# Performance work log

Hardware: AMD Instinct MI355X
Metric: run time of the kernel (lower is better)

## Reference

```python
import jax, jax.numpy as jnp
import numpy as np

B = 4096           # batch size
NG = 4096          # num_gene_sets (columns of input)
G = 1024           # number of aggregation groups
GS = 32            # members per group (CSR-packed; code handles ragged too)
T = G * GS         # total flat indices


def setup_inputs() -> dict:
    key = jax.random.key(0)
    k1, k2, k3 = jax.random.split(key, 3)
    gene_set_features = jax.random.normal(k1, (B, NG), dtype=jnp.float32)
    att_weights = jax.random.normal(k2, (T,), dtype=jnp.float32)  # concat of per-group logits
    flat_idx = jax.random.randint(k3, (T,), 0, NG, dtype=jnp.int64)
    segment_ids = (jnp.arange(T, dtype=jnp.int64) // GS)          # sorted group id per entry
    return {
        "gene_set_features": gene_set_features,
        "att_weights": att_weights,
        "flat_idx": flat_idx,
        "segment_ids": segment_ids,
        "num_segments": G,
    }


def reference(gene_set_features, att_weights, flat_idx, segment_ids, num_segments):
    # Per-group (segment) softmax over the batch-independent attention logits.
    seg_max = jax.ops.segment_max(att_weights, segment_ids, num_segments=num_segments)
    ex = jnp.exp(att_weights - seg_max[segment_ids])
    denom = jax.ops.segment_sum(ex, segment_ids, num_segments=num_segments)
    attn = ex / denom[segment_ids]                     # (T,) softmax weights per group
    # Gather all group members for every batch row in one shot, weight, segment-sum.
    gathered = gene_set_features[:, flat_idx]          # (B, T)
    weighted = gathered * attn[None, :]                # (B, T)
    out = jax.ops.segment_sum(weighted.T, segment_ids, num_segments=num_segments).T  # (B, G)
    return out
```

## Files before the change

kernel.cpp:

```cpp
#include <hip/hip_runtime.h>

#define NGK 4096
#define BK 4096
#define GK 1024
#define GSK 32
#define TK (GK * GSK)

#define BTILE 4
#define AGG_THREADS 512

__global__ __launch_bounds__(256) void seg_softmax_kernel(
        const float* __restrict__ att,
        const int*   __restrict__ idx,
        unsigned*    __restrict__ pairs) {
    int t = blockIdx.x * 256 + threadIdx.x;
    float w = att[t];

    float m = w;
    #pragma unroll
    for (int d = 16; d >= 1; d >>= 1) m = fmaxf(m, __shfl_xor(m, d, 32));
    float e = expf(w - m);
    float s = e;
    #pragma unroll
    for (int d = 16; d >= 1; d >>= 1) s += __shfl_xor(s, d, 32);

    unsigned uw = __float_as_uint(e / s);
    uw = (uw + 0x7fffu + ((uw >> 16) & 1u)) & 0xffff0000u;

    int g = t >> 5;
    int j = t & 31;
    pairs[((j >> 2) * GK + g) * 4 + (j & 3)] = uw | ((unsigned)idx[t] << 4);
}

__global__ __launch_bounds__(AGG_THREADS, 8) void agg_kernel(
        const float* __restrict__ F,
        const uint4* __restrict__ pairs4,
        float*       __restrict__ out) {
    __shared__ float4 lds4[NGK];

    const int tid = threadIdx.x;
    const int b0 = blockIdx.x * BTILE;

    #pragma unroll
    for (int it = 0; it < NGK / AGG_THREADS; ++it) {
        int c = tid + it * AGG_THREADS;
        float4 v;
        v.x = F[(b0 + 0) * NGK + c];
        v.y = F[(b0 + 1) * NGK + c];
        v.z = F[(b0 + 2) * NGK + c];
        v.w = F[(b0 + 3) * NGK + c];
        lds4[c] = v;
    }
    __syncthreads();

    const char* ldsb = reinterpret_cast<const char*>(lds4);

    #pragma unroll
    for (int k = 0; k < GK / AGG_THREADS; ++k) {
        int g = tid + k * AGG_THREADS;
        float a0 = 0.f, a1 = 0.f, a2 = 0.f, a3 = 0.f;
        #pragma unroll 2
        for (int jj = 0; jj < GSK / 4; ++jj) {
            uint4 u = pairs4[jj * GK + g];
            #pragma unroll
            for (int c = 0; c < 4; ++c) {
                unsigned uc = (c == 0) ? u.x : (c == 1) ? u.y : (c == 2) ? u.z : u.w;
                const float4 q = *reinterpret_cast<const float4*>(ldsb + (uc & 0xfff0u));
                float w = __uint_as_float(uc & 0xffff0000u);
                a0 += w * q.x;
                a1 += w * q.y;
                a2 += w * q.z;
                a3 += w * q.w;
            }
        }
        out[(b0 + 0) * GK + g] = a0;
        out[(b0 + 1) * GK + g] = a1;
        out[(b0 + 2) * GK + g] = a2;
        out[(b0 + 3) * GK + g] = a3;
    }
}

extern "C" void kernel_launch(void* const* d_in, const int* in_sizes, int n_in,
                              void* d_out, int out_size, void* d_ws, size_t ws_size,
                              hipStream_t stream) {
    const float* F   = (const float*)d_in[0];
    const float* att = (const float*)d_in[1];
    const int*   idx = (const int*)d_in[2];

    unsigned* pairs = (unsigned*)d_ws;
    float*    out   = (float*)d_out;

    seg_softmax_kernel<<<TK / 256, 256, 0, stream>>>(att, idx, pairs);
    agg_kernel<<<BK / BTILE, AGG_THREADS, 0, stream>>>(F, (const uint4*)pairs, out);
}
```

Measured before the change: 113.6 us.

## Store features in fp16 LDS and accumulate with packed half2 FMAs

Converts the per-block feature tile to fp16 so that each LDS entry holds four batch values in 8 bytes instead of 16. The inner accumulation now uses packed __hfma2 over windows of four group members, and each window's partial sum is folded into fp32 accumulators. The weights are fp16 half2 duplicates packed with byte offsets into 8-byte pairs, and the launch-bounds occupancy hint is dropped. This halves LDS footprint and gather bandwidth and doubles FMA throughput, at the cost of fp16 rounding of the inputs and of the partial sums, which may hurt accuracy.

```diff
diff --git a/kernel.cpp b/kernel.cpp
--- a/kernel.cpp
+++ b/kernel.cpp
@@ -1,4 +1,5 @@
 #include <hip/hip_runtime.h>
+#include <hip/hip_fp16.h>
 
 #define NGK 4096
 #define BK 4096
@@ -9,10 +10,17 @@
 #define BTILE 4
 #define AGG_THREADS 512
 
+__device__ __forceinline__ unsigned h2_bits(__half2 h) {
+    union { __half2 h; unsigned u; } cv; cv.h = h; return cv.u;
+}
+__device__ __forceinline__ __half2 bits_h2(unsigned u) {
+    union { unsigned u; __half2 h; } cv; cv.u = u; return cv.h;
+}
+
 __global__ __launch_bounds__(256) void seg_softmax_kernel(
         const float* __restrict__ att,
         const int*   __restrict__ idx,
-        unsigned*    __restrict__ pairs) {
+        uint2*       __restrict__ pairs2) {
     int t = blockIdx.x * 256 + threadIdx.x;
     float w = att[t];
 
@@ -24,19 +32,21 @@
     #pragma unroll
     for (int d = 16; d >= 1; d >>= 1) s += __shfl_xor(s, d, 32);
 
-    unsigned uw = __float_as_uint(e / s);
-    uw = (uw + 0x7fffu + ((uw >> 16) & 1u)) & 0xffff0000u;
+    float aw = e / s;
+    __half  hw = __float2half(aw);
+    __half2 w2 = __half2half2(hw);
 
     int g = t >> 5;
     int j = t & 31;
-    pairs[((j >> 2) * GK + g) * 4 + (j & 3)] = uw | ((unsigned)idx[t] << 4);
+    pairs2[((j >> 1) * GK + g) * 2 + (j & 1)] =
+        make_uint2(h2_bits(w2), (unsigned)idx[t] << 3);
 }
 
-__global__ __launch_bounds__(AGG_THREADS, 8) void agg_kernel(
+__global__ __launch_bounds__(AGG_THREADS) void agg_kernel(
         const float* __restrict__ F,
-        const uint4* __restrict__ pairs4,
+        const uint4* __restrict__ pq,
         float*       __restrict__ out) {
-    __shared__ float4 lds4[NGK];
+    __shared__ uint2 lds[NGK];
 
     const int tid = threadIdx.x;
     const int b0 = blockIdx.x * BTILE;
@@ -44,34 +54,45 @@
     #pragma unroll
     for (int it = 0; it < NGK / AGG_THREADS; ++it) {
         int c = tid + it * AGG_THREADS;
-        float4 v;
-        v.x = F[(b0 + 0) * NGK + c];
-        v.y = F[(b0 + 1) * NGK + c];
-        v.z = F[(b0 + 2) * NGK + c];
-        v.w = F[(b0 + 3) * NGK + c];
-        lds4[c] = v;
+        float v0 = F[(b0 + 0) * NGK + c];
+        float v1 = F[(b0 + 1) * NGK + c];
+        float v2 = F[(b0 + 2) * NGK + c];
+        float v3 = F[(b0 + 3) * NGK + c];
+        uint2 q;
+        q.x = h2_bits(__floats2half2_rn(v0, v1));
+        q.y = h2_bits(__floats2half2_rn(v2, v3));
+        lds[c] = q;
     }
     __syncthreads();
 
-    const char* ldsb = reinterpret_cast<const char*>(lds4);
+    const char* ldsb = reinterpret_cast<const char*>(lds);
 
     #pragma unroll
-    for (int k = 0; k < GK / AGG_THREADS; ++k) {
-        int g = tid + k * AGG_THREADS;
+    for (int s = 0; s < 2; ++s) {
+        const int g = tid + s * AGG_THREADS;
         float a0 = 0.f, a1 = 0.f, a2 = 0.f, a3 = 0.f;
-        #pragma unroll 2
-        for (int jj = 0; jj < GSK / 4; ++jj) {
-            uint4 u = pairs4[jj * GK + g];
+        #pragma unroll
+        for (int win = 0; win < 8; ++win) {
+            __half2 p01 = __half2half2(__float2half(0.f));
+            __half2 p23 = p01;
             #pragma unroll
-            for (int c = 0; c < 4; ++c) {
-                unsigned uc = (c == 0) ? u.x : (c == 1) ? u.y : (c == 2) ? u.z : u.w;
-                const float4 q = *reinterpret_cast<const float4*>(ldsb + (uc & 0xfff0u));
-                float w = __uint_as_float(uc & 0xffff0000u);
-                a0 += w * q.x;
-                a1 += w * q.y;
-                a2 += w * q.z;
-                a3 += w * q.w;
+            for (int q = 0; q < 2; ++q) {
+                uint4 u = pq[(win * 2 + q) * GK + g];
+                {
+                    uint2 d = *reinterpret_cast<const uint2*>(ldsb + u.y);
+                    __half2 w2 = bits_h2(u.x);
+                    p01 = __hfma2(bits_h2(d.x), w2, p01);
+                    p23 = __hfma2(bits_h2(d.y), w2, p23);
+                }
+                {
+                    uint2 d = *reinterpret_cast<const uint2*>(ldsb + u.w);
+                    __half2 w2 = bits_h2(u.z);
+                    p01 = __hfma2(bits_h2(d.x), w2, p01);
+                    p23 = __hfma2(bits_h2(d.y), w2, p23);
+                }
             }
+            a0 += __low2float(p01);  a1 += __high2float(p01);
+            a2 += __low2float(p23);  a3 += __high2float(p23);
         }
         out[(b0 + 0) * GK + g] = a0;
         out[(b0 + 1) * GK + g] = a1;
@@ -87,9 +108,9 @@
     const float* att = (const float*)d_in[1];
     const int*   idx = (const int*)d_in[2];
 
-    unsigned* pairs = (unsigned*)d_ws;
-    float*    out   = (float*)d_out;
+    uint2* pairs2 = (uint2*)d_ws;
+    float* out    = (float*)d_out;
 
-    seg_softmax_kernel<<<TK / 256, 256, 0, stream>>>(att, idx, pairs);
-    agg_kernel<<<BK / BTILE, AGG_THREADS, 0, stream>>>(F, (const uint4*)pairs, out);
+    seg_softmax_kernel<<<TK / 256, 256, 0, stream>>>(att, idx, pairs2);
+    agg_kernel<<<BK / BTILE, AGG_THREADS, 0, stream>>>(F, (const uint4*)pairs2, out);
 }
```

New measurement: 117.3 us. 3.3% more time.
